# Kernel tuning notes

Hardware: AMD Instinct MI355X
Metric: run time of the kernel (lower is better)

## Reference

```python
import jax, jax.numpy as jnp
import numpy as np
import math

B, L, E, H = 4, 4096, 2048, 16
HD = E // H  # 128

def setup_inputs() -> dict:
    key = jax.random.key(0)
    k1, k2, k3, k4, k5 = jax.random.split(key, 5)
    s = 1.0 / math.sqrt(E)
    return {
        "x": jax.random.normal(k1, (B, L, E), dtype=jnp.float32),
        "Wq": jax.random.normal(k2, (E, E), dtype=jnp.float32) * s,
        "bq": jax.random.normal(k3, (E,), dtype=jnp.float32) * s,
        "Wkv": jax.random.normal(k4, (2 * HD, E), dtype=jnp.float32) * s,
        "bkv": jax.random.normal(k5, (2 * HD,), dtype=jnp.float32) * s,
    }

def reference(x, Wq, bq, Wkv, bkv):
    b, l, e = x.shape
    hd = Wkv.shape[0] // 2
    h = e // hd
    q = (x @ Wq.T + bq).reshape(b, l, h, hd)          # [B,L,H,hd]
    kv = (x @ Wkv.T + bkv).reshape(b, l, 2, hd)
    k, v = kv[:, :, 0], kv[:, :, 1]                   # [B,L,hd] each
    # Faithful to source: q @ k.unsqueeze(2).transpose(-2,-1) -> [B,L,H,1]
    attn = jnp.einsum('blhd,bld->blh', q, k)[..., None] / math.sqrt(hd)
    attn = jax.nn.softmax(attn, axis=-1)              # size-1 axis -> all ones
    # attn @ v.unsqueeze(2): [B,L,H,1] @ [B,L,1,hd] -> [B,L,H,hd]
    out = (attn * v[:, :, None, :]).reshape(b, l, -1)  # [B,L,E]
    return out
```

## Files before the change

### kernel.cpp

```cpp
#include <hip/hip_runtime.h>


typedef __attribute__((ext_vector_type(8))) short bf16x8;
typedef __attribute__((ext_vector_type(4))) float f32x4;

#define M_TOTAL 16384
#define K_DIM   2048
#define N_DIM   128
#define BM      16
#define BK      64
#define NT      (K_DIM / BK)
#define THREADS 256

__device__ __forceinline__ unsigned short f2bf(float f) {
    unsigned int u = __float_as_uint(f);
    u += 0x7FFFu + ((u >> 16) & 1u);
    return (unsigned short)(u >> 16);
}

__global__ void prep_wv(const float* __restrict__ Wkv, unsigned short* __restrict__ Wv) {
    int i = blockIdx.x * blockDim.x + threadIdx.x;
    const float4 f = reinterpret_cast<const float4*>(Wkv + N_DIM * K_DIM)[i];
    ushort4 o;
    o.x = f2bf(f.x); o.y = f2bf(f.y); o.z = f2bf(f.z); o.w = f2bf(f.w);
    reinterpret_cast<ushort4*>(Wv)[i] = o;
}

__global__ __launch_bounds__(THREADS) void mqa_v_gemm(
    const float* __restrict__ x,
    const unsigned short* __restrict__ Wv,
    const float* __restrict__ bkv,
    float* __restrict__ out)
{
    __shared__ __align__(16) unsigned short A_lds[2][BM * BK];
    __shared__ __align__(16) float v_lds[BM][132];

    const int tid  = threadIdx.x;
    const int lane = tid & 63;
    const int wave = tid >> 6;
    const size_t row0 = (size_t)blockIdx.x * BM;

    const int srow = tid >> 4;
    const int skc  = (tid & 15) << 2;
    const float* xp = x + (row0 + srow) * K_DIM + skc;
    const int swz_byte = srow * 128 + (((skc << 1)) ^ ((srow & 7) << 4));

    const int frow = lane & 15;
    const int fg   = lane >> 4;
    const int a_byte0 = frow * 128 + (((fg << 4)      ) ^ ((frow & 7) << 4));
    const int a_byte1 = frow * 128 + (((fg << 4) | 64 ) ^ ((frow & 7) << 4));

    const unsigned short* wp0 = Wv + (wave * 32 +  0 + frow) * K_DIM + (fg << 3);
    const unsigned short* wp1 = Wv + (wave * 32 + 16 + frow) * K_DIM + (fg << 3);

    float4 stg = *reinterpret_cast<const float4*>(xp);
    {
        ushort4 u = { f2bf(stg.x), f2bf(stg.y), f2bf(stg.z), f2bf(stg.w) };
        *reinterpret_cast<ushort4*>(reinterpret_cast<char*>(A_lds[0]) + swz_byte) = u;
    }
    __syncthreads();

    f32x4 acc0 = {0.f, 0.f, 0.f, 0.f};
    f32x4 acc1 = {0.f, 0.f, 0.f, 0.f};

    for (int t = 0; t < NT; ++t) {
        const int cur = t & 1;
        if (t + 1 < NT)
            stg = *reinterpret_cast<const float4*>(xp + (t + 1) * BK);

        const char* ab = reinterpret_cast<const char*>(A_lds[cur]);
        bf16x8 a0 = *reinterpret_cast<const bf16x8*>(ab + a_byte0);
        bf16x8 a1 = *reinterpret_cast<const bf16x8*>(ab + a_byte1);

        const int k0 = t * BK;
        bf16x8 b00 = *reinterpret_cast<const bf16x8*>(wp0 + k0);
        bf16x8 b10 = *reinterpret_cast<const bf16x8*>(wp1 + k0);
        bf16x8 b01 = *reinterpret_cast<const bf16x8*>(wp0 + k0 + 32);
        bf16x8 b11 = *reinterpret_cast<const bf16x8*>(wp1 + k0 + 32);

        acc0 = __builtin_amdgcn_mfma_f32_16x16x32_bf16(a0, b00, acc0, 0, 0, 0);
        acc1 = __builtin_amdgcn_mfma_f32_16x16x32_bf16(a0, b10, acc1, 0, 0, 0);
        acc0 = __builtin_amdgcn_mfma_f32_16x16x32_bf16(a1, b01, acc0, 0, 0, 0);
        acc1 = __builtin_amdgcn_mfma_f32_16x16x32_bf16(a1, b11, acc1, 0, 0, 0);

        if (t + 1 < NT) {
            ushort4 u = { f2bf(stg.x), f2bf(stg.y), f2bf(stg.z), f2bf(stg.w) };
            *reinterpret_cast<ushort4*>(reinterpret_cast<char*>(A_lds[cur ^ 1]) + swz_byte) = u;
        }
        __syncthreads();
    }

    const int c0 = wave * 32 + frow;
    const int c1 = c0 + 16;
    const float bias0 = bkv[N_DIM + c0];
    const float bias1 = bkv[N_DIM + c1];
    #pragma unroll
    for (int j = 0; j < 4; ++j) {
        const int r = fg * 4 + j;
        v_lds[r][c0] = acc0[j] + bias0;
        v_lds[r][c1] = acc1[j] + bias1;
    }
    __syncthreads();

    float4* op = reinterpret_cast<float4*>(out + row0 * K_DIM);
    for (int i = tid; i < BM * (K_DIM / 4); i += THREADS) {
        const int r  = i >> 9;
        const int c4 = i & 31;
        op[i] = *reinterpret_cast<const float4*>(&v_lds[r][c4 << 2]);
    }
}

extern "C" void kernel_launch(void* const* d_in, const int* in_sizes, int n_in,
                              void* d_out, int out_size, void* d_ws, size_t ws_size,
                              hipStream_t stream)
{
    const float* x   = (const float*)d_in[0];
    const float* Wkv = (const float*)d_in[3];
    const float* bkv = (const float*)d_in[4];
    float* out       = (float*)d_out;
    unsigned short* Wv = (unsigned short*)d_ws;

    prep_wv<<<(N_DIM * K_DIM / 4) / 256, 256, 0, stream>>>(Wkv, Wv);
    mqa_v_gemm<<<M_TOTAL / BM, THREADS, 0, stream>>>(x, Wv, bkv, out);
}
```

Baseline: 299.2 us.

## Stream x and prepacked Wv into LDS via async global_load_lds with 4-stage pipeline

Rewrites the V-projection GEMM main loop so that fp32 x tiles and a pre-packed, MFMA-fragment-ordered bf16 Wv are copied straight into LDS using global_load_lds. A 4-buffer ring keeps two tiles in flight, synchronised with explicit vmcnt waits and barriers. The fp32-to-bf16 conversion for A moves to the LDS read side using v_cvt_pk_bf16_f32. This is meant to hide global load latency and drop the register staging round trip, at the cost of about 80KB of LDS per block, which limits occupancy.

```diff
diff --git a/kernel.cpp b/kernel.cpp
--- a/kernel.cpp
+++ b/kernel.cpp
@@ -6,11 +6,11 @@
 
 #define M_TOTAL 16384
 #define K_DIM   2048
-#define N_DIM   128
 #define BM      16
 #define BK      64
 #define NT      (K_DIM / BK)
-#define THREADS 256
+#define TILE_BYTES 20480
+#define NBUF    4
 
 __device__ __forceinline__ unsigned short f2bf(float f) {
     unsigned int u = __float_as_uint(f);
@@ -18,95 +18,122 @@
     return (unsigned short)(u >> 16);
 }
 
-__global__ void prep_wv(const float* __restrict__ Wkv, unsigned short* __restrict__ Wv) {
-    int i = blockIdx.x * blockDim.x + threadIdx.x;
-    const float4 f = reinterpret_cast<const float4*>(Wkv + N_DIM * K_DIM)[i];
-    ushort4 o;
-    o.x = f2bf(f.x); o.y = f2bf(f.y); o.z = f2bf(f.z); o.w = f2bf(f.w);
-    reinterpret_cast<ushort4*>(Wv)[i] = o;
+#define GLOAD_LDS16(gp, lp) __builtin_amdgcn_global_load_lds( \
+    (const __attribute__((address_space(1))) void*)(gp),      \
+    (__attribute__((address_space(3))) void*)(lp), 16, 0, 0)
+
+#define WAITV(N) asm volatile("s_waitcnt vmcnt(" #N ")" ::: "memory")
+#define BAR() do { asm volatile("" ::: "memory"); __builtin_amdgcn_s_barrier(); \
+                   asm volatile("" ::: "memory"); } while (0)
+
+__global__ void prep_wv(const float* __restrict__ Wkv, unsigned short* __restrict__ Wvp) {
+    const int tid = blockIdx.x * 256 + threadIdx.x;
+    const int l  = tid & 63;
+    const int cb = (tid >> 6) & 15;
+    const int t  = tid >> 10;
+    const int c  = cb & 7, ks = cb >> 3;
+    const int col   = c * 16 + (l & 15);
+    const int kbase = t * 64 + ks * 32 + (l >> 4) * 8;
+    const float* src = Wkv + (size_t)(128 + col) * K_DIM + kbase;
+    const float4 f0 = *reinterpret_cast<const float4*>(src);
+    const float4 f1 = *reinterpret_cast<const float4*>(src + 4);
+    ushort4 o0 = { f2bf(f0.x), f2bf(f0.y), f2bf(f0.z), f2bf(f0.w) };
+    ushort4 o1 = { f2bf(f1.x), f2bf(f1.y), f2bf(f1.z), f2bf(f1.w) };
+    ushort4* dst = reinterpret_cast<ushort4*>(Wvp + (size_t)tid * 8);
+    dst[0] = o0; dst[1] = o1;
 }
 
-__global__ __launch_bounds__(THREADS) void mqa_v_gemm(
+__global__ __launch_bounds__(256, 2) void mqa_v_gemm(
     const float* __restrict__ x,
-    const unsigned short* __restrict__ Wv,
+    const unsigned short* __restrict__ Wvp,
     const float* __restrict__ bkv,
     float* __restrict__ out)
 {
-    __shared__ __align__(16) unsigned short A_lds[2][BM * BK];
-    __shared__ __align__(16) float v_lds[BM][132];
+    __shared__ __align__(16) char smem[NBUF * TILE_BYTES];
 
     const int tid  = threadIdx.x;
-    const int lane = tid & 63;
-    const int wave = tid >> 6;
+    const int l    = tid & 63;
+    const int w    = tid >> 6;
+    const int frow = l & 15;
+    const int fg   = l >> 4;
     const size_t row0 = (size_t)blockIdx.x * BM;
 
-    const int srow = tid >> 4;
-    const int skc  = (tid & 15) << 2;
-    const float* xp = x + (row0 + srow) * K_DIM + skc;
-    const int swz_byte = srow * 128 + (((skc << 1)) ^ ((srow & 7) << 4));
+    const int srow   = w * 4 + (l >> 4);
+    const int scol16 = frow ^ (srow & 7);
+    const float* gA = x + (row0 + srow) * K_DIM + scol16 * 4;
 
-    const int frow = lane & 15;
-    const int fg   = lane >> 4;
-    const int a_byte0 = frow * 128 + (((fg << 4)      ) ^ ((frow & 7) << 4));
-    const int a_byte1 = frow * 128 + (((fg << 4) | 64 ) ^ ((frow & 7) << 4));
-
-    const unsigned short* wp0 = Wv + (wave * 32 +  0 + frow) * K_DIM + (fg << 3);
-    const unsigned short* wp1 = Wv + (wave * 32 + 16 + frow) * K_DIM + (fg << 3);
-
-    float4 stg = *reinterpret_cast<const float4*>(xp);
-    {
-        ushort4 u = { f2bf(stg.x), f2bf(stg.y), f2bf(stg.z), f2bf(stg.w) };
-        *reinterpret_cast<ushort4*>(reinterpret_cast<char*>(A_lds[0]) + swz_byte) = u;
-    }
-    __syncthreads();
+    #define STAGE(t, buf) do {                                            \
+        char* tb_ = smem + (buf) * TILE_BYTES;                            \
+        GLOAD_LDS16(gA + (t) * BK, tb_ + w * 1024);                       \
+        const unsigned short* gb_ = Wvp + (size_t)(t) * 8192 + w * 512 + l * 8; \
+        GLOAD_LDS16(gb_,        tb_ + 4096 + (w     ) * 1024);            \
+        GLOAD_LDS16(gb_ + 2048, tb_ + 4096 + (w +  4) * 1024);            \
+        GLOAD_LDS16(gb_ + 4096, tb_ + 4096 + (w +  8) * 1024);            \
+        GLOAD_LDS16(gb_ + 6144, tb_ + 4096 + (w + 12) * 1024);            \
+    } while (0)
 
     f32x4 acc0 = {0.f, 0.f, 0.f, 0.f};
     f32x4 acc1 = {0.f, 0.f, 0.f, 0.f};
 
-    for (int t = 0; t < NT; ++t) {
-        const int cur = t & 1;
-        if (t + 1 < NT)
-            stg = *reinterpret_cast<const float4*>(xp + (t + 1) * BK);
+    #define COMPUTE(t) do {                                               \
+        const char* tb_ = smem + ((t) & (NBUF - 1)) * TILE_BYTES;         \
+        const char* Ab_ = tb_;                                            \
+        const char* Bb_ = tb_ + 4096;                                     \
+        _Pragma("unroll")                                                 \
+        for (int ks = 0; ks < 2; ++ks) {                                  \
+            float4 af0 = *reinterpret_cast<const float4*>(                \
+                Ab_ + frow * 256 + (((ks * 8 + fg * 2 + 0) ^ (frow & 7)) << 4)); \
+            float4 af1 = *reinterpret_cast<const float4*>(                \
+                Ab_ + frow * 256 + (((ks * 8 + fg * 2 + 1) ^ (frow & 7)) << 4)); \
+            union { unsigned int u[4]; bf16x8 v; } a_;                    \
+            asm("v_cvt_pk_bf16_f32 %0, %1, %2" : "=v"(a_.u[0]) : "v"(af0.x), "v"(af0.y)); \
+            asm("v_cvt_pk_bf16_f32 %0, %1, %2" : "=v"(a_.u[1]) : "v"(af0.z), "v"(af0.w)); \
+            asm("v_cvt_pk_bf16_f32 %0, %1, %2" : "=v"(a_.u[2]) : "v"(af1.x), "v"(af1.y)); \
+            asm("v_cvt_pk_bf16_f32 %0, %1, %2" : "=v"(a_.u[3]) : "v"(af1.z), "v"(af1.w)); \
+            bf16x8 b0 = *reinterpret_cast<const bf16x8*>(                 \
+                Bb_ + (ks * 8 + 2 * w    ) * 1024 + l * 16);              \
+            bf16x8 b1 = *reinterpret_cast<const bf16x8*>(                 \
+                Bb_ + (ks * 8 + 2 * w + 1) * 1024 + l * 16);              \
+            acc0 = __builtin_amdgcn_mfma_f32_16x16x32_bf16(a_.v, b0, acc0, 0, 0, 0); \
+            acc1 = __builtin_amdgcn_mfma_f32_16x16x32_bf16(a_.v, b1, acc1, 0, 0, 0); \
+        }                                                                 \
+    } while (0)
 
-        const char* ab = reinterpret_cast<const char*>(A_lds[cur]);
-        bf16x8 a0 = *reinterpret_cast<const bf16x8*>(ab + a_byte0);
-        bf16x8 a1 = *reinterpret_cast<const bf16x8*>(ab + a_byte1);
+    STAGE(0, 0);
+    STAGE(1, 1);
 
-        const int k0 = t * BK;
-        bf16x8 b00 = *reinterpret_cast<const bf16x8*>(wp0 + k0);
-        bf16x8 b10 = *reinterpret_cast<const bf16x8*>(wp1 + k0);
-        bf16x8 b01 = *reinterpret_cast<const bf16x8*>(wp0 + k0 + 32);
-        bf16x8 b11 = *reinterpret_cast<const bf16x8*>(wp1 + k0 + 32);
+    for (int t = 0; t < NT - 2; ++t) {
+        STAGE(t + 2, (t + 2) & (NBUF - 1));
+        WAITV(10);
+        BAR();
+        COMPUTE(t);
+    }
+    WAITV(5);
+    BAR();
+    COMPUTE(NT - 2);
+    WAITV(0);
+    BAR();
+    COMPUTE(NT - 1);
 
-        acc0 = __builtin_amdgcn_mfma_f32_16x16x32_bf16(a0, b00, acc0, 0, 0, 0);
-        acc1 = __builtin_amdgcn_mfma_f32_16x16x32_bf16(a0, b10, acc1, 0, 0, 0);
-        acc0 = __builtin_amdgcn_mfma_f32_16x16x32_bf16(a1, b01, acc0, 0, 0, 0);
-        acc1 = __builtin_amdgcn_mfma_f32_16x16x32_bf16(a1, b11, acc1, 0, 0, 0);
-
-        if (t + 1 < NT) {
-            ushort4 u = { f2bf(stg.x), f2bf(stg.y), f2bf(stg.z), f2bf(stg.w) };
-            *reinterpret_cast<ushort4*>(reinterpret_cast<char*>(A_lds[cur ^ 1]) + swz_byte) = u;
-        }
-        __syncthreads();
-    }
-
-    const int c0 = wave * 32 + frow;
+    float* vl = reinterpret_cast<float*>(smem);
+    const int c0 = w * 32 + frow;
     const int c1 = c0 + 16;
-    const float bias0 = bkv[N_DIM + c0];
-    const float bias1 = bkv[N_DIM + c1];
+    const float bias0 = bkv[128 + c0];
+    const float bias1 = bkv[128 + c1];
     #pragma unroll
     for (int j = 0; j < 4; ++j) {
         const int r = fg * 4 + j;
-        v_lds[r][c0] = acc0[j] + bias0;
-        v_lds[r][c1] = acc1[j] + bias1;
+        vl[r * 132 + c0] = acc0[j] + bias0;
+        vl[r * 132 + c1] = acc1[j] + bias1;
     }
     __syncthreads();
 
     float4* op = reinterpret_cast<float4*>(out + row0 * K_DIM);
-    for (int i = tid; i < BM * (K_DIM / 4); i += THREADS) {
+    #pragma unroll
+    for (int i = tid; i < BM * (K_DIM / 4); i += 256) {
         const int r  = i >> 9;
-        const int c4 = i & 31;
-        op[i] = *reinterpret_cast<const float4*>(&v_lds[r][c4 << 2]);
+        const int c4 = i & 511;
+        op[i] = *reinterpret_cast<const float4*>(vl + r * 132 + (c4 & 31) * 4);
     }
 }
 
@@ -118,8 +145,8 @@
     const float* Wkv = (const float*)d_in[3];
     const float* bkv = (const float*)d_in[4];
     float* out       = (float*)d_out;
-    unsigned short* Wv = (unsigned short*)d_ws;
+    unsigned short* Wvp = (unsigned short*)d_ws;
 
-    prep_wv<<<(N_DIM * K_DIM / 4) / 256, 256, 0, stream>>>(Wkv, Wv);
-    mqa_v_gemm<<<M_TOTAL / BM, THREADS, 0, stream>>>(x, Wv, bkv, out);
+    prep_wv<<<128, 256, 0, stream>>>(Wkv, Wvp);
+    mqa_v_gemm<<<M_TOTAL / BM, 256, 0, stream>>>(x, Wvp, bkv, out);
 }
```

Result: faster. 266.3 us (-11.0%).
